# Kernel tuning notes

Hardware: AMD Instinct MI355X
Metric: run time of the kernel (lower is better)

The kernel has to match this reference:

```python
import jax, jax.numpy as jnp
import numpy as np

B = 256      # graph pairs
N = 256      # nodes per graph (uniform -> padding is a reshape)
DEG = 16     # avg degree
D = 32       # one_hot_dim
F1, F2, F3 = 128, 64, 64
T = 16       # tensor_neurons
BINS = 16
BOT = 16     # bottle_neck_neurons


def setup_inputs() -> dict:
    key = jax.random.key(0)
    ks = jax.random.split(key, 24)
    NT = B * N            # total nodes per side
    NE = B * N * DEG      # total directed edges per side
    x_q = jax.random.normal(ks[0], (NT, D), jnp.float32)
    x_c = jax.random.normal(ks[1], (NT, D), jnp.float32)
    edge_q = jax.random.randint(ks[2], (2, NE), 0, NT, jnp.int32)
    edge_c = jax.random.randint(ks[3], (2, NE), 0, NT, jnp.int32)
    qgraph_sizes = jnp.full((B,), N, jnp.int32)
    cgraph_sizes = jnp.full((B,), N, jnp.int32)

    def glorot(k, shape):
        fan = sum(shape[-2:]) if len(shape) >= 2 else shape[0] * 2
        return jax.random.uniform(k, shape, jnp.float32, -1.0, 1.0) * np.sqrt(6.0 / fan)

    params = dict(
        W1=glorot(ks[4], (D, F1)), b1=jnp.zeros((F1,), jnp.float32),
        W2=glorot(ks[5], (F1, F2)), b2=jnp.zeros((F2,), jnp.float32),
        W3=glorot(ks[6], (F2, F3)), b3=jnp.zeros((F3,), jnp.float32),
        attn_w=glorot(ks[7], (F3, F3)),
        ntn_a_w=glorot(ks[8], (T, F3, F3)),
        ntn_b_w=glorot(ks[9], (2 * F3, T)),
        ntn_bias=glorot(ks[10], (T, 1)),
        fc1_w=glorot(ks[11], (T + BINS, BOT)), fc1_b=jnp.zeros((BOT,), jnp.float32),
        fc2_w=glorot(ks[12], (BOT, 1)), fc2_b=jnp.zeros((1,), jnp.float32),
    )
    return dict(x_q=x_q, edge_q=edge_q, x_c=x_c, edge_c=edge_c,
                qgraph_sizes=qgraph_sizes, cgraph_sizes=cgraph_sizes, **params)


def _gcn(x, src, dst, W, b):
    n = x.shape[0]
    h = x @ W
    loop = jnp.arange(n, dtype=src.dtype)
    s = jnp.concatenate([src, loop])
    d = jnp.concatenate([dst, loop])
    deg = jax.ops.segment_sum(jnp.ones(s.shape, h.dtype), d, num_segments=n)
    dinv = jnp.where(deg > 0, jax.lax.rsqrt(jnp.maximum(deg, 1.0)), 0.0)
    coef = (dinv[s] * dinv[d])[:, None]
    return jax.ops.segment_sum(h[s] * coef, d, num_segments=n) + b


def _gnn(x, ei, W1, b1, W2, b2, W3, b3):
    src, dst = ei[0], ei[1]
    h = jax.nn.relu(_gcn(x, src, dst, W1, b1))        # dropout is identity in eval
    h = jax.nn.relu(_gcn(h, src, dst, W2, b2))
    return _gcn(h, src, dst, W3, b3)                  # [B*N, F3]


def _att_pool(q, attn_w, sizes):
    # q: [B, N, F3]
    ctx = jnp.tanh((q.sum(axis=1) @ attn_w) / sizes.astype(q.dtype)[:, None])  # [B, F3]
    sig = jax.nn.sigmoid(jnp.einsum('bnf,bf->bn', q, ctx))                      # [B, N]
    return jnp.einsum('bnf,bn->bf', q, sig)                                     # [B, F3]


def _pair_hist(q, c):
    # per-pair histogram of q @ c^T with BINS bins over each pair's [min, max]
    s = jax.lax.stop_gradient(jnp.einsum('bnf,bmf->bnm', q, c))  # [B, N, N]
    mn = s.min(axis=(1, 2), keepdims=True)
    mx = s.max(axis=(1, 2), keepdims=True)
    idx = jnp.clip(jnp.floor((s - mn) / jnp.maximum(mx - mn, 1e-12) * BINS),
                   0, BINS - 1).astype(jnp.int32)
    gid = (idx + jnp.arange(B, dtype=jnp.int32)[:, None, None] * BINS).reshape(-1)
    h = jax.ops.segment_sum(jnp.ones(gid.shape, jnp.float32), gid,
                            num_segments=B * BINS).reshape(B, BINS)
    return h / h.sum(axis=1, keepdims=True)


def reference(x_q, edge_q, x_c, edge_c, qgraph_sizes, cgraph_sizes,
              W1, b1, W2, b2, W3, b3, attn_w, ntn_a_w, ntn_b_w, ntn_bias,
              fc1_w, fc1_b, fc2_w, fc2_b):
    q = _gnn(x_q, edge_q, W1, b1, W2, b2, W3, b3).reshape(B, N, F3)
    c = _gnn(x_c, edge_c, W1, b1, W2, b2, W3, b3).reshape(B, N, F3)
    e1 = _att_pool(q, attn_w, qgraph_sizes)
    e2 = _att_pool(c, attn_w, cgraph_sizes)
    ntn = (jnp.einsum('bi,tij,bj->bt', e1, ntn_a_w, e2)
           + jnp.concatenate([e1, e2], axis=-1) @ ntn_b_w
           + ntn_bias[:, 0])
    scores = jax.nn.relu(ntn)                                   # [B, T]
    hist = _pair_hist(q, c)                                     # [B, BINS]
    scores = jnp.concatenate([scores, hist], axis=1)
    scores = jax.nn.relu(scores @ fc1_w + fc1_b)
    p = jax.nn.sigmoid(scores @ fc2_w + fc2_b)[:, 0]            # [B]
    ged = -0.5 * (qgraph_sizes + cgraph_sizes).astype(p.dtype) * jnp.log(p)
    return ged
```

## Files before the change

### kernel.cpp

```cpp
#include <hip/hip_runtime.h>
#include <hip/hip_bf16.h>
#include <math.h>

#define BB 256
#define NN 256
#define NT (BB*NN)
#define NT2 (2*NT)
#define NE (NT*16)
#define DD 32
#define F1C 128
#define F2C 64
#define F3C 64
#define TT 16
#define BINS 16

#define NBUCK 256
#define BSHIFT 9
#define BNODES 512
#define BCAP 10240
#define EPB 4096

typedef __attribute__((ext_vector_type(8))) short short8;
typedef __attribute__((ext_vector_type(4))) float f32x4;
typedef __attribute__((ext_vector_type(2))) float f32x2;

__device__ inline float b2f(ushort u) { return __uint_as_float(((uint)u) << 16); }
__device__ inline ushort f2b(float f) {
    uint u = __float_as_uint(f);
    return (ushort)((u + 0x7fffu + ((u >> 16) & 1u)) >> 16);
}
__device__ inline float clamp8(float v) { return fminf(fmaxf(v, -448.0f), 448.0f); }
__device__ inline uchar f2f8(float v) {
    int r = __builtin_amdgcn_cvt_pk_fp8_f32(clamp8(v), 0.0f, 0, false);
    return (uchar)(r & 0xff);
}
__device__ inline void f8x8_acc(uint2 w, float* acc) {
    f32x2 p;
    p = __builtin_amdgcn_cvt_pk_f32_fp8(w.x, false); acc[0] += p.x; acc[1] += p.y;
    p = __builtin_amdgcn_cvt_pk_f32_fp8(w.x, true);  acc[2] += p.x; acc[3] += p.y;
    p = __builtin_amdgcn_cvt_pk_f32_fp8(w.y, false); acc[4] += p.x; acc[5] += p.y;
    p = __builtin_amdgcn_cvt_pk_f32_fp8(w.y, true);  acc[6] += p.x; acc[7] += p.y;
}
__device__ inline uint2 f8x8_pack(const float* v) {
    uint2 r;
    r.x = (uint)__builtin_amdgcn_cvt_pk_fp8_f32(clamp8(v[0]), clamp8(v[1]), 0, false);
    r.x = (uint)__builtin_amdgcn_cvt_pk_fp8_f32(clamp8(v[2]), clamp8(v[3]), (int)r.x, true);
    r.y = (uint)__builtin_amdgcn_cvt_pk_fp8_f32(clamp8(v[4]), clamp8(v[5]), 0, false);
    r.y = (uint)__builtin_amdgcn_cvt_pk_fp8_f32(clamp8(v[6]), clamp8(v[7]), (int)r.y, true);
    return r;
}

__global__ __launch_bounds__(256) void zero_k(int* __restrict__ gcount) {
    gcount[threadIdx.x] = 0;
}

__global__ __launch_bounds__(256) void p1cvt_k(const int* __restrict__ eq, const int* __restrict__ ec,
                                               uint* __restrict__ staged, int* __restrict__ gcount,
                                               const float* __restrict__ W1, const float* __restrict__ W2,
                                               const float* __restrict__ W3, ushort* __restrict__ Wt1,
                                               ushort* __restrict__ Wt2, uchar* __restrict__ Wt3f8) {
    int t = threadIdx.x;
    if (blockIdx.x < 512) {
        __shared__ uint s_pk[EPB];
        __shared__ int s_cnt[NBUCK];
        __shared__ int s_off[NBUCK];
        __shared__ int s_base[NBUCK];
        __shared__ int s_gb[NBUCK];
        bool sideB = blockIdx.x >= 256;
        const int* edge = sideB ? ec : eq;
        int off = sideB ? NT : 0;
        int e0 = (blockIdx.x & 255) * EPB;
        s_cnt[t] = 0;
        __syncthreads();
        uint pk[16]; int bk[16];
#pragma unroll
        for (int j = 0; j < 16; j++) {
            int e = e0 + j * 256 + t;
            int s = edge[e] + off;
            int d = edge[NE + e] + off;
            bk[j] = d >> BSHIFT;
            pk[j] = ((uint)s << BSHIFT) | (uint)(d & (BNODES - 1));
            atomicAdd(&s_cnt[bk[j]], 1);
        }
        __syncthreads();
        s_off[t] = s_cnt[t];
        __syncthreads();
        for (int o = 1; o < NBUCK; o <<= 1) {
            int x = (t >= o) ? s_off[t - o] : 0;
            __syncthreads();
            s_off[t] += x;
            __syncthreads();
        }
        {
            int ex = s_off[t] - s_cnt[t];
            s_base[t] = ex;
            s_off[t] = ex;
            s_gb[t] = atomicAdd(&gcount[t], s_cnt[t]);
        }
        __syncthreads();
#pragma unroll
        for (int j = 0; j < 16; j++) {
            int pos = atomicAdd(&s_off[bk[j]], 1);
            s_pk[pos] = pk[j];
        }
        __syncthreads();
        int w = t >> 6, l = t & 63;
        int bsel = l >> 4, l16 = l & 15;
        for (int pb = w; pb < NBUCK / 4; pb += 4) {
            int bkt = pb * 4 + bsel;
            int n = s_cnt[bkt], st = s_base[bkt], gb = s_gb[bkt];
            if (gb + n > BCAP) n = max(0, BCAP - gb);
            for (int i = l16; i < n; i += 16)
                staged[bkt * BCAP + gb + i] = s_pk[st + i];
        }
    } else {
        int i = (blockIdx.x - 512) * 256 + t;
        if (i < DD * F1C)  { int k = i / F1C, n = i % F1C; Wt1[n * DD + k]  = f2b(W1[i]); }
        if (i < F1C * F2C) { int k = i / F2C, n = i % F2C; Wt2[n * F1C + k] = f2b(W2[i]); }
        if (i < F2C * F3C) { int k = i / F3C, n = i % F3C; Wt3f8[n * F2C + k] = f2f8(W3[i]); }
    }
}

__global__ __launch_bounds__(256) void csr_p2_k(const uint* __restrict__ staged, const int* __restrict__ gcount,
                                                int* __restrict__ rp, int* __restrict__ indeg,
                                                float* __restrict__ dinv, int* __restrict__ ep,
                                                const float* __restrict__ xq, const float* __restrict__ xc,
                                                ushort* __restrict__ xb) {
    int b = blockIdx.x;
    int t = threadIdx.x;
    __shared__ int cnt[BNODES];
    __shared__ int fl[BNODES];
    __shared__ int wsum[256];
    __shared__ int gsc[NBUCK];
    __shared__ float sdv[BNODES];
    cnt[t] = 0; cnt[t + 256] = 0;
    gsc[t] = min(gcount[t], BCAP);
    __syncthreads();
    for (int off = 1; off < NBUCK; off <<= 1) {
        int x = (t >= off) ? gsc[t - off] : 0;
        __syncthreads();
        gsc[t] += x;
        __syncthreads();
    }
    int gbase = (b == 0) ? 0 : gsc[b - 1];
    int n = min(gcount[b], BCAP);
    const uint* sb = staged + (size_t)b * BCAP;
    int i = t;
    for (; i + 768 < n; i += 1024) {
        uint p0 = sb[i];
        uint p1 = sb[i + 256];
        uint p2 = sb[i + 512];
        uint p3 = sb[i + 768];
        atomicAdd(&cnt[p0 & (BNODES - 1)], 1);
        atomicAdd(&cnt[p1 & (BNODES - 1)], 1);
        atomicAdd(&cnt[p2 & (BNODES - 1)], 1);
        atomicAdd(&cnt[p3 & (BNODES - 1)], 1);
    }
    for (; i < n; i += 256)
        atomicAdd(&cnt[sb[i] & (BNODES - 1)], 1);
    __syncthreads();
    int base2 = t * 2;
    int c0 = cnt[base2], c1 = cnt[base2 + 1];
    int s2 = c0 + c1;
    wsum[t] = s2;
    __syncthreads();
    for (int off = 1; off < 256; off <<= 1) {
        int x = (t >= off) ? wsum[t - off] : 0;
        __syncthreads();
        wsum[t] += x;
        __syncthreads();
    }
    int p = gbase + wsum[t] - s2;
    int v0 = b * BNODES + base2;
    float d0 = rsqrtf((float)(c0 + 1));
    float d1 = rsqrtf((float)(c1 + 1));
    rp[v0] = p;          fl[base2] = p;
    indeg[v0] = c0;      dinv[v0] = d0;      sdv[base2] = d0;
    p += c0;
    rp[v0 + 1] = p;      fl[base2 + 1] = p;
    indeg[v0 + 1] = c1;  dinv[v0 + 1] = d1;  sdv[base2 + 1] = d1;
    __syncthreads();
    i = t;
    for (; i + 768 < n; i += 1024) {
        uint p0 = sb[i];
        uint p1 = sb[i + 256];
        uint p2 = sb[i + 512];
        uint p3 = sb[i + 768];
        ep[atomicAdd(&fl[p0 & (BNODES - 1)], 1)] = (int)(p0 >> BSHIFT);
        ep[atomicAdd(&fl[p1 & (BNODES - 1)], 1)] = (int)(p1 >> BSHIFT);
        ep[atomicAdd(&fl[p2 & (BNODES - 1)], 1)] = (int)(p2 >> BSHIFT);
        ep[atomicAdd(&fl[p3 & (BNODES - 1)], 1)] = (int)(p3 >> BSHIFT);
    }
    for (; i < n; i += 256) {
        uint pk = sb[i];
        ep[atomicAdd(&fl[pk & (BNODES - 1)], 1)] = (int)(pk >> BSHIFT);
    }
    {
        const float* xs = (b < 128) ? (xq + (size_t)b * BNODES * DD)
                                    : (xc + ((size_t)b * BNODES - NT) * DD);
        ushort* xd = xb + (size_t)b * BNODES * DD;
        for (int g = t; g < BNODES * DD / 4; g += 256) {
            int r = g >> 3;
            float4 v = ((const float4*)xs)[g];
            float dv = sdv[r];
            ushort4 o;
            o.x = f2b(v.x * dv); o.y = f2b(v.y * dv);
            o.z = f2b(v.z * dv); o.w = f2b(v.w * dv);
            ((ushort4*)xd)[g] = o;
        }
    }
}

__global__ __launch_bounds__(256) void agg_bf_k(const ushort* __restrict__ in, const int* __restrict__ rp,
                                                const int* __restrict__ indeg, const int* __restrict__ ep,
                                                const float* __restrict__ dinv,
                                                ushort* __restrict__ out) {
    int g = threadIdx.x >> 2;
    int l = threadIdx.x & 3;
    int v = blockIdx.x * 64 + g;
    float dv = dinv[v];
    short8 rs = *(const short8*)(in + (size_t)v * 32 + l * 8);
    float acc[8];
#pragma unroll
    for (int j = 0; j < 8; j++) acc[j] = b2f((ushort)rs[j]);
    int start = rp[v];
    int cnt   = indeg[v];
    int i = 0;
    for (; i + 4 <= cnt; i += 4) {
        int s0 = ep[start + i];
        int s1 = ep[start + i + 1];
        int s2 = ep[start + i + 2];
        int s3 = ep[start + i + 3];
        short8 r0 = *(const short8*)(in + (size_t)s0 * 32 + l * 8);
        short8 r1 = *(const short8*)(in + (size_t)s1 * 32 + l * 8);
        short8 r2 = *(const short8*)(in + (size_t)s2 * 32 + l * 8);
        short8 r3 = *(const short8*)(in + (size_t)s3 * 32 + l * 8);
#pragma unroll
        for (int j = 0; j < 8; j++) {
            acc[j] += b2f((ushort)r0[j]);
            acc[j] += b2f((ushort)r1[j]);
            acc[j] += b2f((ushort)r2[j]);
            acc[j] += b2f((ushort)r3[j]);
        }
    }
    for (; i < cnt; i++) {
        int s0 = ep[start + i];
        short8 r0 = *(const short8*)(in + (size_t)s0 * 32 + l * 8);
#pragma unroll
        for (int j = 0; j < 8; j++) acc[j] += b2f((ushort)r0[j]);
    }
    short8 o;
#pragma unroll
    for (int j = 0; j < 8; j++) o[j] = (short)f2b(dv * acc[j]);
    *(short8*)(out + (size_t)v * 32 + l * 8) = o;
}

template<bool OUT_BF16, bool BIAS, bool RELU>
__global__ __launch_bounds__(256) void agg_f8_k(const uchar* __restrict__ in, const int* __restrict__ rp,
                                                const int* __restrict__ indeg, const int* __restrict__ ep,
                                                const float* __restrict__ dinv,
                                                const float* __restrict__ bias, void* __restrict__ outp) {
    int g = threadIdx.x >> 3;
    int l = threadIdx.x & 7;
    int v = blockIdx.x * 32 + g;
    float dv = dinv[v];
    float acc[8] = {0, 0, 0, 0, 0, 0, 0, 0};
    f8x8_acc(*(const uint2*)(in + (size_t)v * 64 + l * 8), acc);
    int start = rp[v];
    int cnt   = indeg[v];
    int i = 0;
    for (; i + 8 <= cnt; i += 8) {
        int sx[8];
#pragma unroll
        for (int j = 0; j < 8; j++) sx[j] = ep[start + i + j];
        uint2 gx[8];
#pragma unroll
        for (int j = 0; j < 8; j++) gx[j] = *(const uint2*)(in + (size_t)sx[j] * 64 + l * 8);
#pragma unroll
        for (int j = 0; j < 8; j++) f8x8_acc(gx[j], acc);
    }
    for (; i + 4 <= cnt; i += 4) {
        int s0 = ep[start + i];
        int s1 = ep[start + i + 1];
        int s2 = ep[start + i + 2];
        int s3 = ep[start + i + 3];
        uint2 g0 = *(const uint2*)(in + (size_t)s0 * 64 + l * 8);
        uint2 g1 = *(const uint2*)(in + (size_t)s1 * 64 + l * 8);
        uint2 g2 = *(const uint2*)(in + (size_t)s2 * 64 + l * 8);
        uint2 g3 = *(const uint2*)(in + (size_t)s3 * 64 + l * 8);
        f8x8_acc(g0, acc); f8x8_acc(g1, acc); f8x8_acc(g2, acc); f8x8_acc(g3, acc);
    }
    for (; i < cnt; i++) {
        int s0 = ep[start + i];
        f8x8_acc(*(const uint2*)(in + (size_t)s0 * 64 + l * 8), acc);
    }
#pragma unroll
    for (int j = 0; j < 8; j++) {
        float x = dv * acc[j];
        if (BIAS) x += bias[l * 8 + j];
        if (RELU) x = fmaxf(x, 0.0f);
        acc[j] = x;
    }
    if (OUT_BF16) {
        short8 o;
#pragma unroll
        for (int j = 0; j < 8; j++) o[j] = (short)f2b(acc[j]);
        *(short8*)((ushort*)outp + (size_t)v * 64 + l * 8) = o;
    } else {
        *(uint2*)((uchar*)outp + (size_t)v * 64 + l * 8) = f8x8_pack(acc);
    }
}

__global__ __launch_bounds__(256) void gemm12_k(const ushort* __restrict__ xa,
                                                const ushort* __restrict__ Wt1,
                                                const float* __restrict__ b1,
                                                const ushort* __restrict__ Wt2,
                                                const float* __restrict__ dinv,
                                                uchar* __restrict__ h8a) {
    __shared__ ushort s_h1[128][136];
    int w = threadIdx.x >> 6, lane = threadIdx.x & 63;
    int r16 = lane & 15, quad = lane >> 4, koff = quad * 8;
    size_t rows0 = (size_t)blockIdx.x * 128;

    short8 af1[2];
#pragma unroll
    for (int mt = 0; mt < 2; mt++)
        af1[mt] = *(const short8*)(xa + (rows0 + (w * 2 + mt) * 16 + r16) * 32 + koff);
#pragma unroll
    for (int nt = 0; nt < 8; nt++) {
        short8 bfr = *(const short8*)(Wt1 + (size_t)(nt * 16 + r16) * 32 + koff);
        f32x4 acc[2] = {{0.f,0.f,0.f,0.f},{0.f,0.f,0.f,0.f}};
        acc[0] = __builtin_amdgcn_mfma_f32_16x16x32_bf16(af1[0], bfr, acc[0], 0, 0, 0);
        acc[1] = __builtin_amdgcn_mfma_f32_16x16x32_bf16(af1[1], bfr, acc[1], 0, 0, 0);
        int col = nt * 16 + r16;
        float bc = b1[col];
#pragma unroll
        for (int mt = 0; mt < 2; mt++)
#pragma unroll
            for (int r = 0; r < 4; r++) {
                int rl = (w * 2 + mt) * 16 + quad * 4 + r;
                s_h1[rl][col] = f2b(fmaxf(acc[mt][r] + bc, 0.0f));
            }
    }
    __syncthreads();

    short8 af2[4][2];
#pragma unroll
    for (int kc = 0; kc < 4; kc++)
#pragma unroll
        for (int mt = 0; mt < 2; mt++)
            af2[kc][mt] = *(const short8*)&s_h1[(w * 2 + mt) * 16 + r16][kc * 32 + koff];
    float dvr[2][4];
#pragma unroll
    for (int mt = 0; mt < 2; mt++)
#pragma unroll
        for (int r = 0; r < 4; r++)
            dvr[mt][r] = dinv[rows0 + (w * 2 + mt) * 16 + quad * 4 + r];
#pragma unroll
    for (int nt = 0; nt < 4; nt++) {
        f32x4 acc[2] = {{0.f,0.f,0.f,0.f},{0.f,0.f,0.f,0.f}};
#pragma unroll
        for (int kc = 0; kc < 4; kc++) {
            short8 bfr = *(const short8*)(Wt2 + (size_t)(nt * 16 + r16) * 128 + kc * 32 + koff);
            acc[0] = __builtin_amdgcn_mfma_f32_16x16x32_bf16(af2[kc][0], bfr, acc[0], 0, 0, 0);
            acc[1] = __builtin_amdgcn_mfma_f32_16x16x32_bf16(af2[kc][1], bfr, acc[1], 0, 0, 0);
        }
#pragma unroll
        for (int mt = 0; mt < 2; mt++)
#pragma unroll
            for (int r = 0; r < 4; r++) {
                size_t row = rows0 + (w * 2 + mt) * 16 + quad * 4 + r;
                int col = nt * 16 + r16;
                h8a[row * 64 + col] = f2f8(acc[mt][r] * dvr[mt][r]);
            }
    }
}

__global__ __launch_bounds__(256) void gemm_f8_k(const uchar* __restrict__ A8,
                                                 const uchar* __restrict__ Wt8,
                                                 const float* __restrict__ dinv,
                                                 uchar* __restrict__ out8) {
    int w = threadIdx.x >> 6, lane = threadIdx.x & 63;
    int r16 = lane & 15, koff = (lane >> 4) * 8;
    size_t rows0 = (size_t)blockIdx.x * 128;

    long af[2][2];
#pragma unroll
    for (int kc = 0; kc < 2; kc++)
#pragma unroll
        for (int mt = 0; mt < 2; mt++)
            af[kc][mt] = *(const long*)(A8 + (rows0 + (w * 2 + mt) * 16 + r16) * 64 + kc * 32 + koff);

    float dvr[2][4];
#pragma unroll
    for (int mt = 0; mt < 2; mt++)
#pragma unroll
        for (int r = 0; r < 4; r++)
            dvr[mt][r] = dinv[rows0 + (w * 2 + mt) * 16 + (lane >> 4) * 4 + r];

#pragma unroll
    for (int nt = 0; nt < 4; nt++) {
        f32x4 acc[2] = {{0.f,0.f,0.f,0.f},{0.f,0.f,0.f,0.f}};
#pragma unroll
        for (int kc = 0; kc < 2; kc++) {
            long b = *(const long*)(Wt8 + (size_t)(nt * 16 + r16) * 64 + kc * 32 + koff);
            acc[0] = __builtin_amdgcn_mfma_f32_16x16x32_fp8_fp8(af[kc][0], b, acc[0], 0, 0, 0);
            acc[1] = __builtin_amdgcn_mfma_f32_16x16x32_fp8_fp8(af[kc][1], b, acc[1], 0, 0, 0);
        }
#pragma unroll
        for (int mt = 0; mt < 2; mt++) {
#pragma unroll
            for (int r = 0; r < 4; r++) {
                size_t row = rows0 + (w * 2 + mt) * 16 + (lane >> 4) * 4 + r;
                int col = nt * 16 + (lane & 15);
                out8[row * 64 + col] = f2f8(acc[mt][r] * dvr[mt][r]);
            }
        }
    }
}

__global__ __launch_bounds__(1024) void pool_hist_k(const ushort* __restrict__ fin,
                                                    const int* __restrict__ qsz, const int* __restrict__ csz,
                                                    const float* __restrict__ attn_w,
                                                    float* __restrict__ e_out, float* __restrict__ histp) {
    __shared__ float smemf[18944];
    int t = threadIdx.x;
    int f = t & 63;
    int w = t >> 6;
    if (blockIdx.x < 512) {
        int b = blockIdx.x & 255;
        bool is_c = blockIdx.x >= BB;
        const ushort* emb = fin + (size_t)blockIdx.x * NN * F3C;
        float size = (float)((is_c ? csz : qsz)[b]);
        float* eo = e_out + (is_c ? BB * F3C : 0) + b * F3C;
        float (*s_emb)[F3C + 1] = (float(*)[F3C + 1])smemf;
        float* s_red = smemf + 16640;
        float* s_sq  = s_red + 1024;
        float* s_ctx = s_sq + 64;
        float* s_sig = s_ctx + 64;
#pragma unroll
        for (int it = 0; it < 2; it++) {
            int idx = it * 8192 + t * 8;
            int row = idx >> 6, f0 = idx & 63;
            short8 v = *(const short8*)(emb + idx);
#pragma unroll
            for (int j = 0; j < 8; j++) s_emb[row][f0 + j] = b2f((ushort)v[j]);
        }
        __syncthreads();
        float psum = 0.0f;
#pragma unroll 8
        for (int i2 = 0; i2 < 16; i2++) psum += s_emb[w * 16 + i2][f];
        s_red[w * 64 + f] = psum;
        __syncthreads();
        if (w == 0) {
            float s = 0.0f;
#pragma unroll
            for (int j = 0; j < 16; j++) s += s_red[j * 64 + f];
            s_sq[f] = s;
            float acc = 0.0f;
            for (int k = 0; k < 64; k++) acc += s_sq[k] * attn_w[k * 64 + f];
            s_ctx[f] = tanhf(acc / size);
        }
        __syncthreads();
        if (t < 256) {
            float acc = 0.0f;
#pragma unroll 8
            for (int k = 0; k < 64; k++) acc += s_emb[t][k] * s_ctx[k];
            s_sig[t] = 1.0f / (1.0f + expf(-acc));
        }
        __syncthreads();
        float eacc = 0.0f;
#pragma unroll 8
        for (int i = 0; i < 16; i++) {
            int n = w * 16 + i;
            eacc += s_sig[n] * s_emb[n][f];
        }
        s_red[w * 64 + f] = eacc;
        __syncthreads();
        if (w == 0) {
            float s = 0.0f;
#pragma unroll
            for (int j = 0; j < 16; j++) s += s_red[j * 64 + f];
            eo[f] = s;
        }
    } else {
        int b = blockIdx.x - 512;
        const ushort* qb = fin + (size_t)b * NN * 64;
        const ushort* cb = fin + (size_t)(NT + b * NN) * 64;
        int lane = t & 63;
        int r16 = lane & 15, koff = (lane >> 4) * 8;
        ushort (*cb_s)[72] = (ushort(*)[72])smemf;
        ushort* h = (ushort*)(smemf + 9216);
        int* hp = (int*)(smemf + 9216 + 8192);
        float* smn = smemf + 9216 + 8192 + 1024;
        float* smx = smn + 16;
        float* s_sc = smx + 16;

#pragma unroll
        for (int it = 0; it < 2; it++) {
            int idx = it * 8192 + t * 8;
            int row = idx >> 6, f0 = idx & 63;
            *(short8*)&cb_s[row][f0] = *(const short8*)(cb + idx);
        }
        short8 a[2];
        {
            int qrow = w * 16 + r16;
#pragma unroll
            for (int kk = 0; kk < 2; kk++)
                a[kk] = *(const short8*)(qb + qrow * 64 + kk * 32 + koff);
        }
        __syncthreads();
        float mn = 1e30f, mx = -1e30f;
        for (int mt = 0; mt < 16; mt++) {
            int crow = mt * 16 + r16;
            short8 b0 = *(const short8*)&cb_s[crow][koff];
            short8 b1 = *(const short8*)&cb_s[crow][32 + koff];
            f32x4 acc = {0.0f, 0.0f, 0.0f, 0.0f};
            acc = __builtin_amdgcn_mfma_f32_16x16x32_bf16(a[0], b0, acc, 0, 0, 0);
            acc = __builtin_amdgcn_mfma_f32_16x16x32_bf16(a[1], b1, acc, 0, 0, 0);
            mn = fminf(mn, fminf(fminf(acc[0], acc[1]), fminf(acc[2], acc[3])));
            mx = fmaxf(mx, fmaxf(fmaxf(acc[0], acc[1]), fmaxf(acc[2], acc[3])));
        }
        for (int off = 32; off; off >>= 1) {
            mn = fminf(mn, __shfl_xor(mn, off, 64));
            mx = fmaxf(mx, __shfl_xor(mx, off, 64));
        }
        if (lane == 0) { smn[w] = mn; smx[w] = mx; }
        __syncthreads();
        if (t == 0) {
            float m0 = smn[0], m1 = smx[0];
#pragma unroll
            for (int j = 1; j < 16; j++) {
                m0 = fminf(m0, smn[j]);
                m1 = fmaxf(m1, smx[j]);
            }
            s_sc[0] = m0;
            s_sc[1] = 16.0f / fmaxf(m1 - m0, 1e-12f);
        }
#pragma unroll
        for (int i = 0; i < 16; i++) h[i * 1024 + t] = 0;
        __syncthreads();
        float bmn = s_sc[0], bscale = s_sc[1];
        for (int mt = 0; mt < 16; mt++) {
            int crow = mt * 16 + r16;
            short8 b0 = *(const short8*)&cb_s[crow][koff];
            short8 b1 = *(const short8*)&cb_s[crow][32 + koff];
            f32x4 acc = {0.0f, 0.0f, 0.0f, 0.0f};
            acc = __builtin_amdgcn_mfma_f32_16x16x32_bf16(a[0], b0, acc, 0, 0, 0);
            acc = __builtin_amdgcn_mfma_f32_16x16x32_bf16(a[1], b1, acc, 0, 0, 0);
#pragma unroll
            for (int r = 0; r < 4; r++) {
                int bin = (int)floorf((acc[r] - bmn) * bscale);
                bin = min(max(bin, 0), 15);
                h[bin * 1024 + t] += 1;
            }
        }
        __syncthreads();
        int bb = t >> 6, part = t & 63;
        int sum = 0;
#pragma unroll
        for (int j = 0; j < 16; j++) sum += (int)h[bb * 1024 + part * 16 + j];
        hp[bb * 64 + part] = sum;
        __syncthreads();
        if (t < 16) {
            int s = 0;
#pragma unroll
            for (int j = 0; j < 64; j++) s += hp[t * 64 + j];
            histp[b * 16 + t] = (float)s;
        }
    }
}

__global__ __launch_bounds__(256) void ntn_final_k(const float* __restrict__ e, const float* __restrict__ A,
                                                   const float* __restrict__ bw, const float* __restrict__ bias,
                                                   const float* __restrict__ histp,
                                                   const float* __restrict__ fc1w, const float* __restrict__ fc1b,
                                                   const float* __restrict__ fc2w, const float* __restrict__ fc2b,
                                                   const int* __restrict__ qsz, const int* __restrict__ csz,
                                                   float* __restrict__ out) {
    int b = blockIdx.x;
    int t = threadIdx.x;
    int lane = t & 63, w = t >> 6;
    __shared__ float s_e1[64], s_e2[64];
    __shared__ float s_ntn[16];
    __shared__ float s_s[32];
    __shared__ float s_a[16];
    if (t < 64) s_e1[t] = e[b * 64 + t];
    else if (t < 128) s_e2[t - 64] = e[BB * 64 + b * 64 + (t - 64)];
    __syncthreads();
#pragma unroll
    for (int r = 0; r < 4; r++) {
        int idx = t + r * 256;
        const float4* Ar = (const float4*)(A + (size_t)idx * 64);
        float acc = 0.0f;
#pragma unroll
        for (int j = 0; j < 16; j++) {
            float4 a4 = Ar[j];
            acc += a4.x * s_e2[4 * j] + a4.y * s_e2[4 * j + 1]
                 + a4.z * s_e2[4 * j + 2] + a4.w * s_e2[4 * j + 3];
        }
        float p = s_e1[lane] * acc;
        for (int off = 32; off; off >>= 1) p += __shfl_xor(p, off, 64);
        if (lane == 0) s_ntn[w + 4 * r] = p;
    }
    __syncthreads();
    if (t < 16) {
        float acc = s_ntn[t] + bias[t];
        for (int k = 0; k < 64; k++) acc += s_e1[k] * bw[k * 16 + t];
        for (int k = 0; k < 64; k++) acc += s_e2[k] * bw[(64 + k) * 16 + t];
        s_s[t] = fmaxf(acc, 0.0f);
        s_s[16 + t] = histp[b * 16 + t] * (1.0f / 65536.0f);
    }
    __syncthreads();
    if (t < 16) {
        float a = fc1b[t];
        for (int k = 0; k < 32; k++) a += s_s[k] * fc1w[k * 16 + t];
        s_a[t] = fmaxf(a, 0.0f);
    }
    __syncthreads();
    if (t == 0) {
        float z = fc2b[0];
        for (int j = 0; j < 16; j++) z += s_a[j] * fc2w[j];
        float nz = -z;
        float sp = (nz > 20.0f) ? nz : log1pf(expf(nz));
        out[b] = 0.5f * (float)(qsz[b] + csz[b]) * sp;
    }
}

extern "C" void kernel_launch(void* const* d_in, const int* in_sizes, int n_in,
                              void* d_out, int out_size, void* d_ws, size_t ws_size,
                              hipStream_t stream) {
    const float* x_q    = (const float*)d_in[0];
    const int*   edge_q = (const int*)d_in[1];
    const float* x_c    = (const float*)d_in[2];
    const int*   edge_c = (const int*)d_in[3];
    const int*   qsz    = (const int*)d_in[4];
    const int*   csz    = (const int*)d_in[5];
    const float* W1 = (const float*)d_in[6];
    const float* b1 = (const float*)d_in[7];
    const float* W2 = (const float*)d_in[8];
    const float* b2 = (const float*)d_in[9];
    const float* W3 = (const float*)d_in[10];
    const float* b3 = (const float*)d_in[11];
    const float* attn_w  = (const float*)d_in[12];
    const float* ntn_a   = (const float*)d_in[13];
    const float* ntn_b   = (const float*)d_in[14];
    const float* ntn_bias= (const float*)d_in[15];
    const float* fc1w = (const float*)d_in[16];
    const float* fc1b = (const float*)d_in[17];
    const float* fc2w = (const float*)d_in[18];
    const float* fc2b = (const float*)d_in[19];
    float* out = (float*)d_out;

    char* w = (char*)d_ws;
    auto alloc = [&](size_t bytes) -> void* {
        void* p = (void*)w;
        w += (bytes + 255) & ~(size_t)255;
        return p;
    };
    int*    rp     = (int*)alloc((size_t)NT2 * 4);
    int*    indeg  = (int*)alloc((size_t)NT2 * 4);
    float*  dinv   = (float*)alloc((size_t)NT2 * 4);
    int*    gcount = (int*)alloc(NBUCK * 4);
    uint*   staged = (uint*)alloc((size_t)NBUCK * BCAP * 4);
    int*    ep     = (int*)alloc((size_t)2 * NE * 4);
    ushort* xb     = (ushort*)alloc((size_t)NT2 * 32 * 2);
    ushort* xa     = (ushort*)alloc((size_t)NT2 * 32 * 2);
    uchar*  h8a    = (uchar*)alloc((size_t)NT2 * 64);
    uchar*  h8b    = (uchar*)alloc((size_t)NT2 * 64);
    ushort* fin    = (ushort*)alloc((size_t)NT2 * 64 * 2);
    ushort* Wt1    = (ushort*)alloc((size_t)DD * F1C * 2);
    ushort* Wt2    = (ushort*)alloc((size_t)F1C * F2C * 2);
    uchar*  Wt3f8  = (uchar*)alloc((size_t)F2C * F3C);
    float*  e12    = (float*)alloc(2 * BB * 64 * 4);
    float*  histp  = (float*)alloc(256 * 16 * 4);

    zero_k<<<1, 256, 0, stream>>>(gcount);
    p1cvt_k<<<512 + 32, 256, 0, stream>>>(edge_q, edge_c, staged, gcount,
                                          W1, W2, W3, Wt1, Wt2, Wt3f8);
    csr_p2_k<<<NBUCK, 256, 0, stream>>>(staged, gcount, rp, indeg, dinv, ep,
                                        x_q, x_c, xb);

    agg_bf_k<<<NT2 / 64, 256, 0, stream>>>(xb, rp, indeg, ep, dinv, xa);
    gemm12_k<<<NT2 / 128, 256, 0, stream>>>(xa, Wt1, b1, Wt2, dinv, h8a);
    agg_f8_k<false, true, true><<<NT2 / 32, 256, 0, stream>>>(h8a, rp, indeg, ep, dinv, b2, h8b);
    gemm_f8_k<<<NT2 / 128, 256, 0, stream>>>(h8b, Wt3f8, dinv, h8a);
    agg_f8_k<true, true, false><<<NT2 / 32, 256, 0, stream>>>(h8a, rp, indeg, ep, dinv, b3, fin);

    pool_hist_k<<<768, 1024, 0, stream>>>(fin, qsz, csz, attn_w, e12, histp);
    ntn_final_k<<<BB, 256, 0, stream>>>(e12, ntn_a, ntn_b, ntn_bias, histp,
                                        fc1w, fc1b, fc2w, fc2b, qsz, csz, out);
}
```

Before: 278.1 us.

## Fuse pooling, histogram and NTN head into a single per-pair tail kernel

Merges the attention-pooling/histogram kernel and the NTN/final MLP kernel into one kernel with one 1024-thread block per graph pair. The block loads both q and c embeddings into shared memory once, computes the histogram, both pooled embeddings and the final score without global intermediates. This removes a kernel launch and the e12/histp round-trips, but serializes the q pooling, c pooling and histogram work within one block and reduces the grid from 768 to 256 blocks.

New measurement: 275.8 us (median of 2 runs). About the same (-0.8%).

```diff
diff --git a/kernel.cpp b/kernel.cpp
--- a/kernel.cpp
+++ b/kernel.cpp
@@ -419,37 +419,113 @@
     }
 }
 
-__global__ __launch_bounds__(1024) void pool_hist_k(const ushort* __restrict__ fin,
-                                                    const int* __restrict__ qsz, const int* __restrict__ csz,
-                                                    const float* __restrict__ attn_w,
-                                                    float* __restrict__ e_out, float* __restrict__ histp) {
-    __shared__ float smemf[18944];
+__global__ __launch_bounds__(1024) void tail_k(const ushort* __restrict__ fin,
+                                               const int* __restrict__ qsz, const int* __restrict__ csz,
+                                               const float* __restrict__ attn_w,
+                                               const float* __restrict__ A, const float* __restrict__ bw,
+                                               const float* __restrict__ ntn_bias,
+                                               const float* __restrict__ fc1w, const float* __restrict__ fc1b,
+                                               const float* __restrict__ fc2w, const float* __restrict__ fc2b,
+                                               float* __restrict__ out) {
+    __shared__ ushort q_s[256][72];
+    __shared__ ushort c_s[256][72];
+    __shared__ ushort h[16 * 1024];
+    __shared__ int hp[16 * 64];
+    __shared__ float s_red[16 * 64];
+    __shared__ float s_sq[64], s_ctx[64], s_sig[256];
+    __shared__ float smn[16], smx[16], s_sc[2];
+    __shared__ float s_e1[64], s_e2[64];
+    __shared__ float s_ntn[16], s_s[32], s_a[16];
+    __shared__ int s_hist[16];
+
+    int b = blockIdx.x;
     int t = threadIdx.x;
     int f = t & 63;
     int w = t >> 6;
-    if (blockIdx.x < 512) {
-        int b = blockIdx.x & 255;
-        bool is_c = blockIdx.x >= BB;
-        const ushort* emb = fin + (size_t)blockIdx.x * NN * F3C;
-        float size = (float)((is_c ? csz : qsz)[b]);
-        float* eo = e_out + (is_c ? BB * F3C : 0) + b * F3C;
-        float (*s_emb)[F3C + 1] = (float(*)[F3C + 1])smemf;
-        float* s_red = smemf + 16640;
-        float* s_sq  = s_red + 1024;
-        float* s_ctx = s_sq + 64;
-        float* s_sig = s_ctx + 64;
-#pragma unroll
-        for (int it = 0; it < 2; it++) {
-            int idx = it * 8192 + t * 8;
-            int row = idx >> 6, f0 = idx & 63;
-            short8 v = *(const short8*)(emb + idx);
-#pragma unroll
-            for (int j = 0; j < 8; j++) s_emb[row][f0 + j] = b2f((ushort)v[j]);
-        }
-        __syncthreads();
+    int r16 = f & 15, koff = (f >> 4) * 8;
+    const ushort* qb = fin + (size_t)b * NN * 64;
+    const ushort* cb = fin + (size_t)(NT + b * NN) * 64;
+
+#pragma unroll
+    for (int it = 0; it < 2; it++) {
+        int idx = it * 8192 + t * 8;
+        int row = idx >> 6, f0 = idx & 63;
+        *(short8*)&q_s[row][f0] = *(const short8*)(qb + idx);
+        *(short8*)&c_s[row][f0] = *(const short8*)(cb + idx);
+    }
+    __syncthreads();
+
+    short8 a[2];
+    {
+        int qrow = w * 16 + r16;
+        a[0] = *(const short8*)&q_s[qrow][koff];
+        a[1] = *(const short8*)&q_s[qrow][32 + koff];
+    }
+    float mn = 1e30f, mx = -1e30f;
+    for (int mt = 0; mt < 16; mt++) {
+        int crow = mt * 16 + r16;
+        short8 b0 = *(const short8*)&c_s[crow][koff];
+        short8 b1 = *(const short8*)&c_s[crow][32 + koff];
+        f32x4 acc = {0.0f, 0.0f, 0.0f, 0.0f};
+        acc = __builtin_amdgcn_mfma_f32_16x16x32_bf16(a[0], b0, acc, 0, 0, 0);
+        acc = __builtin_amdgcn_mfma_f32_16x16x32_bf16(a[1], b1, acc, 0, 0, 0);
+        mn = fminf(mn, fminf(fminf(acc[0], acc[1]), fminf(acc[2], acc[3])));
+        mx = fmaxf(mx, fmaxf(fmaxf(acc[0], acc[1]), fmaxf(acc[2], acc[3])));
+    }
+    for (int off = 32; off; off >>= 1) {
+        mn = fminf(mn, __shfl_xor(mn, off, 64));
+        mx = fmaxf(mx, __shfl_xor(mx, off, 64));
+    }
+    if (f == 0) { smn[w] = mn; smx[w] = mx; }
+    __syncthreads();
+    if (t == 0) {
+        float m0 = smn[0], m1 = smx[0];
+#pragma unroll
+        for (int j = 1; j < 16; j++) {
+            m0 = fminf(m0, smn[j]);
+            m1 = fmaxf(m1, smx[j]);
+        }
+        s_sc[0] = m0;
+        s_sc[1] = 16.0f / fmaxf(m1 - m0, 1e-12f);
+    }
+#pragma unroll
+    for (int i = 0; i < 16; i++) h[i * 1024 + t] = 0;
+    __syncthreads();
+    float bmn = s_sc[0], bscale = s_sc[1];
+    for (int mt = 0; mt < 16; mt++) {
+        int crow = mt * 16 + r16;
+        short8 b0 = *(const short8*)&c_s[crow][koff];
+        short8 b1 = *(const short8*)&c_s[crow][32 + koff];
+        f32x4 acc = {0.0f, 0.0f, 0.0f, 0.0f};
+        acc = __builtin_amdgcn_mfma_f32_16x16x32_bf16(a[0], b0, acc, 0, 0, 0);
+        acc = __builtin_amdgcn_mfma_f32_16x16x32_bf16(a[1], b1, acc, 0, 0, 0);
+#pragma unroll
+        for (int r = 0; r < 4; r++) {
+            int bin = (int)floorf((acc[r] - bmn) * bscale);
+            bin = min(max(bin, 0), 15);
+            h[bin * 1024 + t] += 1;
+        }
+    }
+    __syncthreads();
+    {
+        int bb = t >> 6, part = t & 63;
+        int sum = 0;
+#pragma unroll
+        for (int j = 0; j < 16; j++) sum += (int)h[bb * 1024 + part * 16 + j];
+        hp[bb * 64 + part] = sum;
+    }
+    __syncthreads();
+    if (t < 16) {
+        int s = 0;
+#pragma unroll
+        for (int j = 0; j < 64; j++) s += hp[t * 64 + j];
+        s_hist[t] = s;
+    }
+
+    {
         float psum = 0.0f;
 #pragma unroll 8
-        for (int i2 = 0; i2 < 16; i2++) psum += s_emb[w * 16 + i2][f];
+        for (int i2 = 0; i2 < 16; i2++) psum += b2f(q_s[w * 16 + i2][f]);
         s_red[w * 64 + f] = psum;
         __syncthreads();
         if (w == 0) {
@@ -459,13 +535,13 @@
             s_sq[f] = s;
             float acc = 0.0f;
             for (int k = 0; k < 64; k++) acc += s_sq[k] * attn_w[k * 64 + f];
-            s_ctx[f] = tanhf(acc / size);
+            s_ctx[f] = tanhf(acc / (float)qsz[b]);
         }
         __syncthreads();
         if (t < 256) {
             float acc = 0.0f;
 #pragma unroll 8
-            for (int k = 0; k < 64; k++) acc += s_emb[t][k] * s_ctx[k];
+            for (int k = 0; k < 64; k++) acc += b2f(q_s[t][k]) * s_ctx[k];
             s_sig[t] = 1.0f / (1.0f + expf(-acc));
         }
         __syncthreads();
@@ -473,7 +549,7 @@
 #pragma unroll 8
         for (int i = 0; i < 16; i++) {
             int n = w * 16 + i;
-            eacc += s_sig[n] * s_emb[n][f];
+            eacc += s_sig[n] * b2f(q_s[n][f]);
         }
         s_red[w * 64 + f] = eacc;
         __syncthreads();
@@ -481,117 +557,53 @@
             float s = 0.0f;
 #pragma unroll
             for (int j = 0; j < 16; j++) s += s_red[j * 64 + f];
-            eo[f] = s;
-        }
-    } else {
-        int b = blockIdx.x - 512;
-        const ushort* qb = fin + (size_t)b * NN * 64;
-        const ushort* cb = fin + (size_t)(NT + b * NN) * 64;
-        int lane = t & 63;
-        int r16 = lane & 15, koff = (lane >> 4) * 8;
-        ushort (*cb_s)[72] = (ushort(*)[72])smemf;
-        ushort* h = (ushort*)(smemf + 9216);
-        int* hp = (int*)(smemf + 9216 + 8192);
-        float* smn = smemf + 9216 + 8192 + 1024;
-        float* smx = smn + 16;
-        float* s_sc = smx + 16;
-
-#pragma unroll
-        for (int it = 0; it < 2; it++) {
-            int idx = it * 8192 + t * 8;
-            int row = idx >> 6, f0 = idx & 63;
-            *(short8*)&cb_s[row][f0] = *(const short8*)(cb + idx);
-        }
-        short8 a[2];
-        {
-            int qrow = w * 16 + r16;
-#pragma unroll
-            for (int kk = 0; kk < 2; kk++)
-                a[kk] = *(const short8*)(qb + qrow * 64 + kk * 32 + koff);
-        }
-        __syncthreads();
-        float mn = 1e30f, mx = -1e30f;
-        for (int mt = 0; mt < 16; mt++) {
-            int crow = mt * 16 + r16;
-            short8 b0 = *(const short8*)&cb_s[crow][koff];
-            short8 b1 = *(const short8*)&cb_s[crow][32 + koff];
-            f32x4 acc = {0.0f, 0.0f, 0.0f, 0.0f};
-            acc = __builtin_amdgcn_mfma_f32_16x16x32_bf16(a[0], b0, acc, 0, 0, 0);
-            acc = __builtin_amdgcn_mfma_f32_16x16x32_bf16(a[1], b1, acc, 0, 0, 0);
-            mn = fminf(mn, fminf(fminf(acc[0], acc[1]), fminf(acc[2], acc[3])));
-            mx = fmaxf(mx, fmaxf(fmaxf(acc[0], acc[1]), fmaxf(acc[2], acc[3])));
-        }
-        for (int off = 32; off; off >>= 1) {
-            mn = fminf(mn, __shfl_xor(mn, off, 64));
-            mx = fmaxf(mx, __shfl_xor(mx, off, 64));
-        }
-        if (lane == 0) { smn[w] = mn; smx[w] = mx; }
-        __syncthreads();
-        if (t == 0) {
-            float m0 = smn[0], m1 = smx[0];
-#pragma unroll
-            for (int j = 1; j < 16; j++) {
-                m0 = fminf(m0, smn[j]);
-                m1 = fmaxf(m1, smx[j]);
-            }
-            s_sc[0] = m0;
-            s_sc[1] = 16.0f / fmaxf(m1 - m0, 1e-12f);
-        }
-#pragma unroll
-        for (int i = 0; i < 16; i++) h[i * 1024 + t] = 0;
-        __syncthreads();
-        float bmn = s_sc[0], bscale = s_sc[1];
-        for (int mt = 0; mt < 16; mt++) {
-            int crow = mt * 16 + r16;
-            short8 b0 = *(const short8*)&cb_s[crow][koff];
-            short8 b1 = *(const short8*)&cb_s[crow][32 + koff];
-            f32x4 acc = {0.0f, 0.0f, 0.0f, 0.0f};
-            acc = __builtin_amdgcn_mfma_f32_16x16x32_bf16(a[0], b0, acc, 0, 0, 0);
-            acc = __builtin_amdgcn_mfma_f32_16x16x32_bf16(a[1], b1, acc, 0, 0, 0);
-#pragma unroll
-            for (int r = 0; r < 4; r++) {
-                int bin = (int)floorf((acc[r] - bmn) * bscale);
-                bin = min(max(bin, 0), 15);
-                h[bin * 1024 + t] += 1;
-            }
-        }
-        __syncthreads();
-        int bb = t >> 6, part = t & 63;
-        int sum = 0;
-#pragma unroll
-        for (int j = 0; j < 16; j++) sum += (int)h[bb * 1024 + part * 16 + j];
-        hp[bb * 64 + part] = sum;
-        __syncthreads();
-        if (t < 16) {
-            int s = 0;
-#pragma unroll
-            for (int j = 0; j < 64; j++) s += hp[t * 64 + j];
-            histp[b * 16 + t] = (float)s;
-        }
-    }
-}
-
-__global__ __launch_bounds__(256) void ntn_final_k(const float* __restrict__ e, const float* __restrict__ A,
-                                                   const float* __restrict__ bw, const float* __restrict__ bias,
-                                                   const float* __restrict__ histp,
-                                                   const float* __restrict__ fc1w, const float* __restrict__ fc1b,
-                                                   const float* __restrict__ fc2w, const float* __restrict__ fc2b,
-                                                   const int* __restrict__ qsz, const int* __restrict__ csz,
-                                                   float* __restrict__ out) {
-    int b = blockIdx.x;
-    int t = threadIdx.x;
-    int lane = t & 63, w = t >> 6;
-    __shared__ float s_e1[64], s_e2[64];
-    __shared__ float s_ntn[16];
-    __shared__ float s_s[32];
-    __shared__ float s_a[16];
-    if (t < 64) s_e1[t] = e[b * 64 + t];
-    else if (t < 128) s_e2[t - 64] = e[BB * 64 + b * 64 + (t - 64)];
-    __syncthreads();
-#pragma unroll
-    for (int r = 0; r < 4; r++) {
-        int idx = t + r * 256;
-        const float4* Ar = (const float4*)(A + (size_t)idx * 64);
+            s_e1[f] = s;
+        }
+    }
+    __syncthreads();
+
+    {
+        float psum = 0.0f;
+#pragma unroll 8
+        for (int i2 = 0; i2 < 16; i2++) psum += b2f(c_s[w * 16 + i2][f]);
+        s_red[w * 64 + f] = psum;
+        __syncthreads();
+        if (w == 0) {
+            float s = 0.0f;
+#pragma unroll
+            for (int j = 0; j < 16; j++) s += s_red[j * 64 + f];
+            s_sq[f] = s;
+            float acc = 0.0f;
+            for (int k = 0; k < 64; k++) acc += s_sq[k] * attn_w[k * 64 + f];
+            s_ctx[f] = tanhf(acc / (float)csz[b]);
+        }
+        __syncthreads();
+        if (t < 256) {
+            float acc = 0.0f;
+#pragma unroll 8
+            for (int k = 0; k < 64; k++) acc += b2f(c_s[t][k]) * s_ctx[k];
+            s_sig[t] = 1.0f / (1.0f + expf(-acc));
+        }
+        __syncthreads();
+        float eacc = 0.0f;
+#pragma unroll 8
+        for (int i = 0; i < 16; i++) {
+            int n = w * 16 + i;
+            eacc += s_sig[n] * b2f(c_s[n][f]);
+        }
+        s_red[w * 64 + f] = eacc;
+        __syncthreads();
+        if (w == 0) {
+            float s = 0.0f;
+#pragma unroll
+            for (int j = 0; j < 16; j++) s += s_red[j * 64 + f];
+            s_e2[f] = s;
+        }
+    }
+    __syncthreads();
+
+    {
+        const float4* Ar = (const float4*)(A + (size_t)t * 64);
         float acc = 0.0f;
 #pragma unroll
         for (int j = 0; j < 16; j++) {
@@ -599,23 +611,23 @@
             acc += a4.x * s_e2[4 * j] + a4.y * s_e2[4 * j + 1]
                  + a4.z * s_e2[4 * j + 2] + a4.w * s_e2[4 * j + 3];
         }
-        float p = s_e1[lane] * acc;
+        float p = s_e1[f] * acc;
         for (int off = 32; off; off >>= 1) p += __shfl_xor(p, off, 64);
-        if (lane == 0) s_ntn[w + 4 * r] = p;
+        if (f == 0) s_ntn[w] = p;
     }
     __syncthreads();
     if (t < 16) {
-        float acc = s_ntn[t] + bias[t];
+        float acc = s_ntn[t] + ntn_bias[t];
         for (int k = 0; k < 64; k++) acc += s_e1[k] * bw[k * 16 + t];
         for (int k = 0; k < 64; k++) acc += s_e2[k] * bw[(64 + k) * 16 + t];
         s_s[t] = fmaxf(acc, 0.0f);
-        s_s[16 + t] = histp[b * 16 + t] * (1.0f / 65536.0f);
+        s_s[16 + t] = (float)s_hist[t] * (1.0f / 65536.0f);
     }
     __syncthreads();
     if (t < 16) {
-        float a = fc1b[t];
-        for (int k = 0; k < 32; k++) a += s_s[k] * fc1w[k * 16 + t];
-        s_a[t] = fmaxf(a, 0.0f);
+        float aa = fc1b[t];
+        for (int k = 0; k < 32; k++) aa += s_s[k] * fc1w[k * 16 + t];
+        s_a[t] = fmaxf(aa, 0.0f);
     }
     __syncthreads();
     if (t == 0) {
@@ -672,8 +684,6 @@
     ushort* Wt1    = (ushort*)alloc((size_t)DD * F1C * 2);
     ushort* Wt2    = (ushort*)alloc((size_t)F1C * F2C * 2);
     uchar*  Wt3f8  = (uchar*)alloc((size_t)F2C * F3C);
-    float*  e12    = (float*)alloc(2 * BB * 64 * 4);
-    float*  histp  = (float*)alloc(256 * 16 * 4);
 
     zero_k<<<1, 256, 0, stream>>>(gcount);
     p1cvt_k<<<512 + 32, 256, 0, stream>>>(edge_q, edge_c, staged, gcount,
@@ -687,7 +697,6 @@
     gemm_f8_k<<<NT2 / 128, 256, 0, stream>>>(h8b, Wt3f8, dinv, h8a);
     agg_f8_k<true, true, false><<<NT2 / 32, 256, 0, stream>>>(h8a, rp, indeg, ep, dinv, b3, fin);
 
-    pool_hist_k<<<768, 1024, 0, stream>>>(fin, qsz, csz, attn_w, e12, histp);
-    ntn_final_k<<<BB, 256, 0, stream>>>(e12, ntn_a, ntn_b, ntn_bias, histp,
-                                        fc1w, fc1b, fc2w, fc2b, qsz, csz, out);
-}
+    tail_k<<<BB, 1024, 0, stream>>>(fin, qsz, csz, attn_w, ntn_a, ntn_b, ntn_bias,
+                                    fc1w, fc1b, fc2w, fc2b, out);
+}
```
